# Kernel tuning notes

Hardware: AMD Instinct MI355X
Metric: run time of the kernel (lower is better)

## Reference

```python
import jax, jax.numpy as jnp
import numpy as np
from math import comb

LEVEL = 16
LENGTH = 64
TOPK = 2
SIZE = 512
BATCH = 32
NEG = -1e8


def _catalan(n_leaves):
    # number of distinct binary trees over n_leaves leaves
    m = n_leaves - 1
    return comb(2 * m, m) // (m + 1)


def _offsets(length, level):
    # cell offset of each chart level: level l occupies (length - l) cells
    return np.cumsum([0] + [length - l for l in range(level)])


def setup_inputs() -> dict:
    key = jax.random.key(0)
    K, B, size, level, length = TOPK, BATCH, SIZE, LEVEL, LENGTH
    L, N = length - level, level
    off = _offsets(length, level)
    ncells = int(off[-1])
    ks = jax.random.split(key, 5)
    chart_h = jax.random.normal(ks[0], (K, B, ncells, size), jnp.float32)
    chart_s = jax.random.normal(ks[1], (K, B, ncells, 1), jnp.float32)
    mat = jax.random.normal(ks[2], (size, size), jnp.float32) / np.sqrt(size).astype(np.float32)
    Wc = jax.random.normal(ks[3], (2 * size, size), jnp.float32) / np.sqrt(2 * size).astype(np.float32)
    bc = jnp.zeros((size,), jnp.float32)
    # structural gather indices: left child = (level n, pos), right child = (level level-1-n, pos+n+1)
    l_idx = np.zeros((L, N), np.int64)
    r_idx = np.zeros((L, N), np.int64)
    for pos in range(L):
        for n in range(N):
            l_idx[pos, n] = off[n] + pos
            r_idx[pos, n] = off[level - 1 - n] + pos + n + 1
    return {
        'chart_h': chart_h, 'chart_s': chart_s,
        'l_index': jnp.asarray(l_idx.reshape(-1)), 'r_index': jnp.asarray(r_idx.reshape(-1)),
        'mat': mat, 'Wc': Wc, 'bc': bc,
    }


def _penalty_mask(level, N, K):
    # Faithful to penalize_incomplete_splits: idx = i // K**2 == 0 for i < K*K,
    # so only the n_idx==0 block is ever penalized. l_level=0, r_level=level-1.
    M = N * K * K
    mask = np.zeros(M, bool)
    for i in range(K * K):
        lk, rk = i // K, i % K
        if _catalan(0 + 1) < lk + 1 or _catalan((level - 1) + 1) < rk + 1:
            mask[i] = True
    return jnp.asarray(mask)


def reference(chart_h, chart_s, l_index, r_index, mat, Wc, bc):
    K, B, ncells, size = chart_h.shape
    level = LEVEL
    N = level
    L = l_index.shape[0] // N
    M = N * K * K
    # gather child states from charts: (K,B,L,N,size) -> (B,L,N,K,size)
    lh = jnp.moveaxis(chart_h[:, :, l_index].reshape(K, B, L, N, size), 0, 3)
    rh = jnp.moveaxis(chart_h[:, :, r_index].reshape(K, B, L, N, size), 0, 3)
    ls = jnp.moveaxis(chart_s[:, :, l_index].reshape(K, B, L, N), 0, 3)  # (B,L,N,K)
    rs = jnp.moveaxis(chart_s[:, :, r_index].reshape(K, B, L, N), 0, 3)
    # bilinear composition score: (B,L,N,K_l,K_r)
    s_raw = jnp.einsum('blnkd,de,blnje->blnkj', lh, mat, rh)
    # flat combo index = n*K*K + lk*K + rk; add child scores
    s = (s_raw + ls[..., :, None] + rs[..., None, :]).reshape(B, L, M)
    s = jnp.where(_penalty_mask(level, N, K), jnp.float32(NEG), s)
    topk_s, topk_idx = jax.lax.top_k(s, K)  # (B,L,K), sorted descending like torch.topk
    # dense compose over all N*K*K combos
    combo_lh = jnp.repeat(lh, K, axis=3).reshape(B, L, M, size)   # lk = z // K
    combo_rh = jnp.tile(rh, (1, 1, 1, K, 1)).reshape(B, L, M, size)  # rk = z % K
    all_h = jnp.tanh(jnp.concatenate([combo_lh, combo_rh], axis=-1) @ Wc + bc)
    topk_h = jnp.take_along_axis(all_h, topk_idx[..., None], axis=2)  # (B,L,K,size)
    # UnitNorm normalize_func
    topk_h = topk_h / jnp.linalg.norm(topk_h, axis=-1, keepdims=True)
    topk_s = topk_s[..., None]  # (B,L,K,1) to match torch shape
    if _catalan(N + 1) < K:  # static no-op at this level
        topk_s = topk_s.at[:, :, _catalan(N + 1):].set(NEG)
    topk_n_idx = topk_idx // (K * K)
    topk_lk = (topk_idx % (K * K)) // K
    topk_rk = (topk_idx % (K * K)) % K
    return topk_h, topk_s, topk_n_idx, topk_lk, topk_rk
```

## Files before the change

kernel.cpp:

```cpp
#include <hip/hip_runtime.h>
#include <cstdint>
#include <cstddef>

#define B_DIM   32
#define L_DIM   48
#define NCELLS  904
#define SZ      512
#define NEGF    (-1e8f)
#define DELTA   0.25f
#define MAXC    32

#define OFF_S   1572864
#define OFF_N   1575936
#define OFF_L   1579008
#define OFF_R   1582080

typedef _Float16  f16x8 __attribute__((ext_vector_type(8)));
typedef float     f32x4 __attribute__((ext_vector_type(4)));

static __device__ __forceinline__ uint16_t f2bf(float f) {
    uint32_t u = __builtin_bit_cast(uint32_t, f);
    u += 0x7fffu + ((u >> 16) & 1u);
    return (uint16_t)(u >> 16);
}

#define GLD16(gp, lp) __builtin_amdgcn_global_load_lds(                        \
        (__attribute__((address_space(1))) void*)(gp),                         \
        (__attribute__((address_space(3))) void*)(lp), 16, 0, 0)

static __device__ __forceinline__ int level_off(int n) {
    return n * 64 - (n * (n - 1)) / 2;
}

__global__ __launch_bounds__(256)
void prep_mat(const float* __restrict__ mat, _Float16* __restrict__ P)
{
    const int tg   = blockIdx.x * 256 + threadIdx.x;
    const int c    = tg >> 6, lane = tg & 63;
    const int srow = 16 * (c & 31) + (lane & 15);
    const int scol = 32 * (c >> 5) + (lane >> 4) * 8;
    const float4 a = *(const float4*)(mat + (size_t)srow * 512 + scol);
    const float4 b = *(const float4*)(mat + (size_t)srow * 512 + scol + 4);
    f16x8 w;
    w[0]=(_Float16)(a.x*64.f); w[1]=(_Float16)(a.y*64.f);
    w[2]=(_Float16)(a.z*64.f); w[3]=(_Float16)(a.w*64.f);
    w[4]=(_Float16)(b.x*64.f); w[5]=(_Float16)(b.y*64.f);
    w[6]=(_Float16)(b.z*64.f); w[7]=(_Float16)(b.w*64.f);
    *(f16x8*)(P + (size_t)tg * 8) = w;
}

__global__ __launch_bounds__(256, 2)
void gemm_fused(const float* __restrict__ A,
                const _Float16* __restrict__ P,
                _Float16* __restrict__ C)
{
    __shared__ _Float16 As16[64 * 512];

    const int t = threadIdx.x;
    const int wave = t >> 6, lane = t & 63;
    const int n0 = blockIdx.x * 256;
    const int nq = n0 >> 4;
    const int m0 = blockIdx.y * 64;
    const int col_l = lane & 15, quad = lane >> 4;

    {
        const int r  = lane;
        const int cw = wave;
        const float* ap = A + (size_t)(m0 + r) * 512 + cw * 128;
        _Float16* drow = As16 + r * 512;
        const int swz = r & 7;
#pragma unroll 2
        for (int s = 0; s < 8; ++s) {
            const f32x4 a0 = *(const f32x4*)(ap + s * 16);
            const f32x4 a1 = *(const f32x4*)(ap + s * 16 + 4);
            const f32x4 a2 = *(const f32x4*)(ap + s * 16 + 8);
            const f32x4 a3 = *(const f32x4*)(ap + s * 16 + 12);
            f16x8 v0, v1;
#pragma unroll
            for (int j = 0; j < 4; ++j) {
                v0[j]     = (_Float16)(a0[j] * 16.f);
                v0[j + 4] = (_Float16)(a1[j] * 16.f);
                v1[j]     = (_Float16)(a2[j] * 16.f);
                v1[j + 4] = (_Float16)(a3[j] * 16.f);
            }
            const int u0 = cw * 16 + s * 2;
            *(f16x8*)&drow[(u0 ^ swz) * 8]       = v0;
            *(f16x8*)&drow[((u0 + 1) ^ swz) * 8] = v1;
        }
    }
    __syncthreads();

    f32x4 acc[4][4];
#pragma unroll
    for (int i = 0; i < 4; ++i)
#pragma unroll
        for (int j = 0; j < 4; ++j) acc[i][j] = (f32x4){0.f, 0.f, 0.f, 0.f};

#pragma unroll 4
    for (int w16 = 0; w16 < 16; ++w16) {
        f16x8 af[4];
#pragma unroll
        for (int mi = 0; mi < 4; ++mi) {
            const int r = mi * 16 + col_l;
            const int u = w16 * 4 + quad;
            af[mi] = *(const f16x8*)&As16[r * 512 + (u ^ (r & 7)) * 8];
        }
#pragma unroll
        for (int ni = 0; ni < 4; ++ni) {
            const int c = w16 * 32 + nq + wave * 4 + ni;
            const f16x8 bf = *(const f16x8*)(P + (size_t)c * 512 + lane * 8);
#pragma unroll
            for (int mi = 0; mi < 4; ++mi)
                acc[mi][ni] = __builtin_amdgcn_mfma_f32_16x16x32_f16(
                    af[mi], bf, acc[mi][ni], 0, 0, 0);
        }
    }

#pragma unroll
    for (int ni = 0; ni < 4; ++ni) {
        const int ncol = n0 + wave * 64 + ni * 16 + col_l;
#pragma unroll
        for (int mi = 0; mi < 4; ++mi) {
            const int mrow = m0 + mi * 16 + quad * 4;
#pragma unroll
            for (int r = 0; r < 4; ++r)
                C[(size_t)(mrow + r) * 512 + ncol] = (_Float16)acc[mi][ni][r];
        }
    }
}

static __device__ __forceinline__ void emit_outputs(
    int row, int i1, int i2, float v1, float v2, float* out)
{
    out[OFF_S + row * 2 + 0] = v1;
    out[OFF_S + row * 2 + 1] = v2;
    out[OFF_N + row * 2 + 0] = (float)(i1 >> 2);
    out[OFF_N + row * 2 + 1] = (float)(i2 >> 2);
    out[OFF_L + row * 2 + 0] = (float)((i1 >> 1) & 1);
    out[OFF_L + row * 2 + 1] = (float)((i2 >> 1) & 1);
    out[OFF_R + row * 2 + 0] = (float)(i1 & 1);
    out[OFF_R + row * 2 + 1] = (float)(i2 & 1);
}

static __device__ __forceinline__ void gather_x(
    int row, int pos, int b, const int* top_z,
    const float* __restrict__ chart_h, uint16_t* __restrict__ X, int tid)
{
#pragma unroll
    for (int kq = 0; kq < 2; ++kq) {
        const int z = top_z[kq];
        const int n = z >> 2, lk = (z >> 1) & 1, rk = z & 1;
        const int lcell = level_off(n) + pos;
        const int rcell = level_off(15 - n) + pos + n + 1;
        const float* srcl = chart_h + ((size_t)(lk * B_DIM + b) * NCELLS + lcell) * SZ;
        const float* srcr = chart_h + ((size_t)(rk * B_DIM + b) * NCELLS + rcell) * SZ;
        uint16_t* dst = X + ((size_t)row * 2 + kq) * 1024;
        const int e = tid * 2;
        const float2 a = *(const float2*)(srcl + e);
        const float2 c = *(const float2*)(srcr + e);
        *(uint32_t*)(dst + e)       = (uint32_t)f2bf(a.x) | ((uint32_t)f2bf(a.y) << 16);
        *(uint32_t*)(dst + 512 + e) = (uint32_t)f2bf(c.x) | ((uint32_t)f2bf(c.y) << 16);
    }
}

__global__ __launch_bounds__(256)
void score_topk(const float* __restrict__ chart_h,
                const _Float16* __restrict__ T16,
                const float* __restrict__ chart_s,
                uint32_t* __restrict__ items,
                int* __restrict__ rowbase,
                int* __restrict__ counter,
                int* __restrict__ flags,
                uint16_t* __restrict__ X,
                float* __restrict__ out)
{
    const int b   = blockIdx.x / L_DIM;
    const int pos = blockIdx.x % L_DIM;
    const int row = blockIdx.x;
    const int wave = threadIdx.x >> 6, lane = threadIdx.x & 63;

    __shared__ float s_sh[64];
    __shared__ int top_z[2];
    __shared__ int flag_sh;

#pragma unroll
    for (int ni = 0; ni < 4; ++ni) {
        const int n = wave * 4 + ni;
        const int lcell = level_off(n) + pos;
        const int rcell = level_off(15 - n) + pos + n + 1;

        const float* lp0 = chart_h + ((size_t)(0 * B_DIM + b) * NCELLS + lcell) * SZ + lane * 8;
        const float* lp1 = chart_h + ((size_t)(1 * B_DIM + b) * NCELLS + lcell) * SZ + lane * 8;
        const float4 l0a = *(const float4*)lp0, l0b = *(const float4*)(lp0 + 4);
        const float4 l1a = *(const float4*)lp1, l1b = *(const float4*)(lp1 + 4);
        const f16x8 t0 = *(const f16x8*)(T16 + ((size_t)(0 * B_DIM + b) * NCELLS + rcell) * SZ + lane * 8);
        const f16x8 t1 = *(const f16x8*)(T16 + ((size_t)(1 * B_DIM + b) * NCELLS + rcell) * SZ + lane * 8);

        float l0[8] = {l0a.x, l0a.y, l0a.z, l0a.w, l0b.x, l0b.y, l0b.z, l0b.w};
        float l1[8] = {l1a.x, l1a.y, l1a.z, l1a.w, l1b.x, l1b.y, l1b.z, l1b.w};

        float d00 = 0.f, d01 = 0.f, d10 = 0.f, d11 = 0.f;
#pragma unroll
        for (int j = 0; j < 8; ++j) {
            const float c0 = (float)t0[j], c1 = (float)t1[j];
            d00 += l0[j] * c0; d01 += l0[j] * c1;
            d10 += l1[j] * c0; d11 += l1[j] * c1;
        }
#pragma unroll
        for (int o = 32; o > 0; o >>= 1) {
            d00 += __shfl_down(d00, o);
            d01 += __shfl_down(d01, o);
            d10 += __shfl_down(d10, o);
            d11 += __shfl_down(d11, o);
        }
        if (lane == 0) {
            const float ls0 = chart_s[(size_t)(0 * B_DIM + b) * NCELLS + lcell];
            const float ls1 = chart_s[(size_t)(1 * B_DIM + b) * NCELLS + lcell];
            const float rs0 = chart_s[(size_t)(0 * B_DIM + b) * NCELLS + rcell];
            const float rs1 = chart_s[(size_t)(1 * B_DIM + b) * NCELLS + rcell];
            const float inv = 1.0f / 1024.0f;
            s_sh[n * 4 + 0] = d00 * inv + ls0 + rs0;
            s_sh[n * 4 + 1] = d01 * inv + ls0 + rs1;
            s_sh[n * 4 + 2] = d10 * inv + ls1 + rs0;
            s_sh[n * 4 + 3] = d11 * inv + ls1 + rs1;
        }
    }
    __syncthreads();

    if (threadIdx.x < 64) {
        float v = s_sh[lane];
        if (lane == 2 || lane == 3) v = NEGF;
        float v1 = v; int i1 = lane;
#pragma unroll
        for (int o = 32; o > 0; o >>= 1) {
            float ov = __shfl_down(v1, o);
            int   oi = __shfl_down(i1, o);
            if (ov > v1 || (ov == v1 && oi < i1)) { v1 = ov; i1 = oi; }
        }
        v1 = __shfl(v1, 0); i1 = __shfl(i1, 0);
        float v2 = (lane == i1) ? -3.4e38f : v; int i2 = lane;
#pragma unroll
        for (int o = 32; o > 0; o >>= 1) {
            float ov = __shfl_down(v2, o);
            int   oi = __shfl_down(i2, o);
            if (ov > v2 || (ov == v2 && oi < i2)) { v2 = ov; i2 = oi; }
        }
        v2 = __shfl(v2, 0); i2 = __shfl(i2, 0);
        float v3 = (lane == i1 || lane == i2) ? -3.4e38f : v;
#pragma unroll
        for (int o = 32; o > 0; o >>= 1) {
            const float ov = __shfl_down(v3, o);
            if (ov > v3) v3 = ov;
        }
        v3 = __shfl(v3, 0);

        const int f = (v1 - v2 < DELTA) || (v2 - v3 < DELTA);
        const bool cand = (v >= v2 - DELTA);
        const unsigned long long mask = __ballot(cand);
        const int nc_full = __popcll(mask);
        const int nc = nc_full < MAXC ? nc_full : MAXC;
        int base = 0;
        if (lane == 0) {
            flags[row] = f ? nc : 0;
            flag_sh = f;
            if (f) base = atomicAdd(counter, nc);
            rowbase[row] = base;
            top_z[0] = i1; top_z[1] = i2;
            if (!f) emit_outputs(row, i1, i2, v1, v2, out);
        }
        base = __shfl(base, 0);
        if (f && cand) {
            const int rank = __popcll(mask & ((1ull << lane) - 1ull));
            if (rank < MAXC) items[base + rank] = ((uint32_t)row << 6) | (uint32_t)lane;
        }
    }
    __syncthreads();

    if (!flag_sh)
        gather_x(row, pos, b, top_z, chart_h, X, threadIdx.x);
}

__global__ __launch_bounds__(256)
void refine_eval(const float* __restrict__ chart_h,
                 const float* __restrict__ chart_s,
                 const float* __restrict__ mat,
                 const uint32_t* __restrict__ items,
                 const int* __restrict__ counter,
                 float* __restrict__ exval)
{
    const int total = *counter;
    const int t = threadIdx.x;
    const int wave = t >> 6, lane = t & 63;

    __shared__ float lh_sh[2][512];
    __shared__ float psum[2][4];

    for (int p = blockIdx.x; 2 * p < total; p += gridDim.x) {
        const int it0 = 2 * p;
        const int it1v = (2 * p + 1 < total);
        const uint32_t item0 = items[it0];
        const uint32_t item1 = it1v ? items[it0 + 1] : item0;

        int rowA = item0 >> 6, zA = item0 & 63;
        int bA = rowA / L_DIM, posA = rowA % L_DIM;
        int nA = zA >> 2, lkA = (zA >> 1) & 1, rkA = zA & 1;
        int lcA = level_off(nA) + posA, rcA = level_off(15 - nA) + posA + nA + 1;
        int rowB = item1 >> 6, zB = item1 & 63;
        int bB = rowB / L_DIM, posB = rowB % L_DIM;
        int nB = zB >> 2, lkB = (zB >> 1) & 1, rkB = zB & 1;
        int lcB = level_off(nB) + posB, rcB = level_off(15 - nB) + posB + nB + 1;

        const float* lhA = chart_h + ((size_t)(lkA * B_DIM + bA) * NCELLS + lcA) * SZ;
        const float* rhA = chart_h + ((size_t)(rkA * B_DIM + bA) * NCELLS + rcA) * SZ;
        const float* lhB = chart_h + ((size_t)(lkB * B_DIM + bB) * NCELLS + lcB) * SZ;
        const float* rhB = chart_h + ((size_t)(rkB * B_DIM + bB) * NCELLS + rcB) * SZ;

        __syncthreads();
        lh_sh[0][t] = lhA[t]; lh_sh[0][t + 256] = lhA[t + 256];
        lh_sh[1][t] = lhB[t]; lh_sh[1][t + 256] = lhB[t + 256];
        const float4 rA0 = *(const float4*)(rhA + lane * 8);
        const float4 rA1 = *(const float4*)(rhA + lane * 8 + 4);
        const float4 rB0 = *(const float4*)(rhB + lane * 8);
        const float4 rB1 = *(const float4*)(rhB + lane * 8 + 4);
        __syncthreads();

        const float* mb = mat + (size_t)(wave * 128) * 512 + lane * 8;
        float a00 = 0.f, a01 = 0.f, b00 = 0.f, b01 = 0.f;
        for (int e = 0; e < 128; e += 2) {
            const float4 m0 = *(const float4*)(mb + (size_t)(e + 0) * 512);
            const float4 m1 = *(const float4*)(mb + (size_t)(e + 0) * 512 + 4);
            const float4 m2 = *(const float4*)(mb + (size_t)(e + 1) * 512);
            const float4 m3 = *(const float4*)(mb + (size_t)(e + 1) * 512 + 4);
            const int eg = wave * 128 + e;
            const float lA0 = lh_sh[0][eg],     lB0 = lh_sh[1][eg];
            const float lA1 = lh_sh[0][eg + 1], lB1 = lh_sh[1][eg + 1];
            const float dA0 = m0.x*rA0.x + m0.y*rA0.y + m0.z*rA0.z + m0.w*rA0.w
                            + m1.x*rA1.x + m1.y*rA1.y + m1.z*rA1.z + m1.w*rA1.w;
            const float dB0 = m0.x*rB0.x + m0.y*rB0.y + m0.z*rB0.z + m0.w*rB0.w
                            + m1.x*rB1.x + m1.y*rB1.y + m1.z*rB1.z + m1.w*rB1.w;
            const float dA1 = m2.x*rA0.x + m2.y*rA0.y + m2.z*rA0.z + m2.w*rA0.w
                            + m3.x*rA1.x + m3.y*rA1.y + m3.z*rA1.z + m3.w*rA1.w;
            const float dB1 = m2.x*rB0.x + m2.y*rB0.y + m2.z*rB0.z + m2.w*rB0.w
                            + m3.x*rB1.x + m3.y*rB1.y + m3.z*rB1.z + m3.w*rB1.w;
            a00 += lA0 * dA0; a01 += lA1 * dA1;
            b00 += lB0 * dB0; b01 += lB1 * dB1;
        }
        float sA = a00 + a01, sB = b00 + b01;
#pragma unroll
        for (int o = 32; o > 0; o >>= 1) {
            sA += __shfl_down(sA, o);
            sB += __shfl_down(sB, o);
        }
        if (lane == 0) { psum[0][wave] = sA; psum[1][wave] = sB; }
        __syncthreads();
        if (t == 0) {
            const float lsA = chart_s[(size_t)(lkA * B_DIM + bA) * NCELLS + lcA];
            const float rsA = chart_s[(size_t)(rkA * B_DIM + bA) * NCELLS + rcA];
            exval[it0] = psum[0][0] + psum[0][1] + psum[0][2] + psum[0][3] + lsA + rsA;
            if (it1v) {
                const float lsB = chart_s[(size_t)(lkB * B_DIM + bB) * NCELLS + lcB];
                const float rsB = chart_s[(size_t)(rkB * B_DIM + bB) * NCELLS + rcB];
                exval[it0 + 1] = psum[1][0] + psum[1][1] + psum[1][2] + psum[1][3] + lsB + rsB;
            }
        }
    }
}

__global__ __launch_bounds__(256)
void refine_pick(const float* __restrict__ chart_h,
                 const uint32_t* __restrict__ items,
                 const int* __restrict__ rowbase,
                 const int* __restrict__ flags,
                 const float* __restrict__ exval,
                 uint16_t* __restrict__ X,
                 float* __restrict__ out)
{
    const int row = blockIdx.x;
    const int nc = flags[row];
    if (nc == 0) return;
    const int b = row / L_DIM, pos = row % L_DIM;
    const int t = threadIdx.x;

    __shared__ int top_z[2];

    if (t == 0) {
        const int base = rowbase[row];
        float v1 = -3.4e38f; int c1 = -1;
        for (int c = 0; c < nc; ++c) {
            const float v = exval[base + c];
            if (v > v1) { v1 = v; c1 = c; }
        }
        float v2 = -3.4e38f; int c2 = -1;
        for (int c = 0; c < nc; ++c) {
            if (c == c1) continue;
            const float v = exval[base + c];
            if (v > v2) { v2 = v; c2 = c; }
        }
        const int i1 = (int)(items[base + c1] & 63u);
        const int i2 = (int)(items[base + c2] & 63u);
        top_z[0] = i1; top_z[1] = i2;
        emit_outputs(row, i1, i2, v1, v2, out);
    }
    __syncthreads();
    gather_x(row, pos, b, top_z, chart_h, X, t);
}

__global__ __launch_bounds__(256)
void transpose_wc(const float* __restrict__ Wc, uint16_t* __restrict__ WcT)
{
    __shared__ float tbuf[64][65];
    const int i0 = blockIdx.x * 64;
    const int o0 = blockIdx.y * 64;
    const int c = threadIdx.x & 63, r4 = threadIdx.x >> 6;
    for (int rr = r4; rr < 64; rr += 4)
        tbuf[rr][c] = Wc[(size_t)(i0 + rr) * 512 + o0 + c];
    __syncthreads();
    for (int rr = r4; rr < 64; rr += 4)
        WcT[(size_t)(o0 + rr) * 1024 + i0 + c] = f2bf(tbuf[c][rr]);
}

typedef __bf16 bf16x8 __attribute__((ext_vector_type(8)));

__global__ __launch_bounds__(256, 2)
void gemm_compose(const uint16_t* __restrict__ A,
                  const uint16_t* __restrict__ Bm,
                  const float* __restrict__ bias,
                  float* __restrict__ C,
                  int M, int Nn, int Kk)
{
    __shared__ uint16_t As[128 * 64];
    __shared__ uint16_t Bs[128 * 64];

    const int tid  = threadIdx.x;
    const int wave = tid >> 6, lane = tid & 63;
    const int m0 = blockIdx.x * 128, n0 = blockIdx.y * 128;
    const int wm = (wave & 1) * 64, wn = (wave >> 1) * 64;
    const int col_l = lane & 15, quad = lane >> 4;
    const int lrow = lane >> 3;
    const int lcol = (lane & 7) * 8;

    f32x4 acc[4][4];
#pragma unroll
    for (int i = 0; i < 4; ++i)
#pragma unroll
        for (int j = 0; j < 4; ++j) acc[i][j] = (f32x4){0.f, 0.f, 0.f, 0.f};

    for (int k0 = 0; k0 < Kk; k0 += 64) {
        __syncthreads();
#pragma unroll
        for (int i = 0; i < 4; ++i) {
            const int q = wave * 4 + i;
            const int r = q * 8 + lrow;
            GLD16(A  + (size_t)(m0 + r) * Kk + k0 + lcol, (char*)As + q * 1024);
            GLD16(Bm + (size_t)(n0 + r) * Kk + k0 + lcol, (char*)Bs + q * 1024);
        }
        __syncthreads();
#pragma unroll
        for (int kk = 0; kk < 64; kk += 32) {
            bf16x8 af[4], bfr[4];
#pragma unroll
            for (int mi = 0; mi < 4; ++mi)
                af[mi] = *(const bf16x8*)&As[(wm + mi * 16 + col_l) * 64 + kk + quad * 8];
#pragma unroll
            for (int ni = 0; ni < 4; ++ni)
                bfr[ni] = *(const bf16x8*)&Bs[(wn + ni * 16 + col_l) * 64 + kk + quad * 8];
#pragma unroll
            for (int mi = 0; mi < 4; ++mi)
#pragma unroll
                for (int ni = 0; ni < 4; ++ni)
                    acc[mi][ni] = __builtin_amdgcn_mfma_f32_16x16x32_bf16(
                        af[mi], bfr[ni], acc[mi][ni], 0, 0, 0);
        }
    }

#pragma unroll
    for (int ni = 0; ni < 4; ++ni) {
        const int ncol = n0 + wn + ni * 16 + col_l;
        const float bv = bias[ncol];
#pragma unroll
        for (int mi = 0; mi < 4; ++mi) {
            const int mrow = m0 + wm + mi * 16 + quad * 4;
#pragma unroll
            for (int r = 0; r < 4; ++r)
                C[(size_t)(mrow + r) * Nn + ncol] = tanhf(acc[mi][ni][r] + bv);
        }
    }
}

__global__ __launch_bounds__(256)
void norm_rows(const float* __restrict__ H, float* __restrict__ out)
{
    const int row = blockIdx.x;
    const float* h = H + (size_t)row * SZ;
    const int t = threadIdx.x;
    const int wave = t >> 6, lane = t & 63;
    const float a = h[t], c = h[t + 256];
    float ss = a * a + c * c;
#pragma unroll
    for (int o = 32; o > 0; o >>= 1) ss += __shfl_down(ss, o);
    __shared__ float wsum[4];
    if (lane == 0) wsum[wave] = ss;
    __syncthreads();
    const float inv = rsqrtf(wsum[0] + wsum[1] + wsum[2] + wsum[3]);
    out[(size_t)row * SZ + t]       = a * inv;
    out[(size_t)row * SZ + t + 256] = c * inv;
}

extern "C" void kernel_launch(void* const* d_in, const int* in_sizes, int n_in,
                              void* d_out, int out_size, void* d_ws, size_t ws_size,
                              hipStream_t stream)
{
    const float* chart_h = (const float*)d_in[0];
    const float* chart_s = (const float*)d_in[1];
    const float* mat = (const float*)d_in[4];
    const float* Wc  = (const float*)d_in[5];
    const float* bc  = (const float*)d_in[6];
    float* out = (float*)d_out;

    char* ws = (char*)d_ws;
    _Float16* T16   = (_Float16*)ws;
    _Float16* MAT16 = (_Float16*)(ws + 59244544);
    uint32_t* ITEMS = (uint32_t*)(ws + 59768832);
    float*    EXVAL = (float*)(ws + 59965440);
    int*      RBASE = (int*)(ws + 60162048);
    int*      CNT   = (int*)(ws + 60168192);
    int*      FLAGS = (int*)(ws + 60168448);
    uint16_t* X     = (uint16_t*)(ws + 60174592);
    uint16_t* WcT   = (uint16_t*)ws;
    float*    H     = (float*)(ws + 1048576);

    hipMemsetAsync(CNT, 0, 4, stream);
    prep_mat<<<dim3(128), 256, 0, stream>>>(mat, MAT16);
    gemm_fused<<<dim3(2, 904), 256, 0, stream>>>(chart_h, MAT16, T16);
    score_topk<<<dim3(B_DIM * L_DIM), 256, 0, stream>>>(chart_h, T16, chart_s,
                                                        ITEMS, RBASE, CNT, FLAGS, X, out);
    transpose_wc<<<dim3(16, 8), 256, 0, stream>>>(Wc, WcT);
    refine_eval<<<dim3(1024), 256, 0, stream>>>(chart_h, chart_s, mat, ITEMS, CNT, EXVAL);
    refine_pick<<<dim3(B_DIM * L_DIM), 256, 0, stream>>>(chart_h, ITEMS, RBASE, FLAGS,
                                                         EXVAL, X, out);
    gemm_compose<<<dim3(24, 4), 256, 0, stream>>>(X, WcT, bc, H, 3072, 512, 1024);
    norm_rows<<<dim3(3072), 256, 0, stream>>>(H, out);
}
```

Measured before the change: 322.2 us.

## Pre-convert chart_h to fp16 once and load it directly into GEMM LDS

Adds a standalone conversion kernel that writes the whole chart_h tensor as scaled fp16 into workspace. The GEMM then fills its LDS tile with direct global-to-LDS loads instead of converting fp32 inside each block, which previously happened twice because of the two column blocks. The scoring kernel also reads fp16 left children, which halves its load bytes. In exchange there is an extra full pass over chart_h (read fp32, write fp16) plus lower score precision, which could change top-k picks near ties.

```diff
diff --git a/kernel.cpp b/kernel.cpp
--- a/kernel.cpp
+++ b/kernel.cpp
@@ -49,8 +49,22 @@
     *(f16x8*)(P + (size_t)tg * 8) = w;
 }
 
+__global__ __launch_bounds__(256)
+void conv_h(const float* __restrict__ x, _Float16* __restrict__ y)
+{
+    const size_t i = ((size_t)blockIdx.x * 256 + threadIdx.x) * 8;
+    const float4 a = *(const float4*)(x + i);
+    const float4 b = *(const float4*)(x + i + 4);
+    f16x8 w;
+    w[0]=(_Float16)(a.x*16.f); w[1]=(_Float16)(a.y*16.f);
+    w[2]=(_Float16)(a.z*16.f); w[3]=(_Float16)(a.w*16.f);
+    w[4]=(_Float16)(b.x*16.f); w[5]=(_Float16)(b.y*16.f);
+    w[6]=(_Float16)(b.z*16.f); w[7]=(_Float16)(b.w*16.f);
+    *(f16x8*)(y + i) = w;
+}
+
 __global__ __launch_bounds__(256, 2)
-void gemm_fused(const float* __restrict__ A,
+void gemm_fused(const _Float16* __restrict__ A16,
                 const _Float16* __restrict__ P,
                 _Float16* __restrict__ C)
 {
@@ -63,30 +77,11 @@
     const int m0 = blockIdx.y * 64;
     const int col_l = lane & 15, quad = lane >> 4;
 
-    {
-        const int r  = lane;
-        const int cw = wave;
-        const float* ap = A + (size_t)(m0 + r) * 512 + cw * 128;
-        _Float16* drow = As16 + r * 512;
-        const int swz = r & 7;
-#pragma unroll 2
-        for (int s = 0; s < 8; ++s) {
-            const f32x4 a0 = *(const f32x4*)(ap + s * 16);
-            const f32x4 a1 = *(const f32x4*)(ap + s * 16 + 4);
-            const f32x4 a2 = *(const f32x4*)(ap + s * 16 + 8);
-            const f32x4 a3 = *(const f32x4*)(ap + s * 16 + 12);
-            f16x8 v0, v1;
-#pragma unroll
-            for (int j = 0; j < 4; ++j) {
-                v0[j]     = (_Float16)(a0[j] * 16.f);
-                v0[j + 4] = (_Float16)(a1[j] * 16.f);
-                v1[j]     = (_Float16)(a2[j] * 16.f);
-                v1[j + 4] = (_Float16)(a3[j] * 16.f);
-            }
-            const int u0 = cw * 16 + s * 2;
-            *(f16x8*)&drow[(u0 ^ swz) * 8]       = v0;
-            *(f16x8*)&drow[((u0 + 1) ^ swz) * 8] = v1;
-        }
+#pragma unroll
+    for (int i = 0; i < 16; ++i) {
+        const int r = wave * 16 + i;
+        GLD16(A16 + (size_t)(m0 + r) * 512 + ((lane ^ (r & 7)) * 8),
+              (char*)As16 + r * 1024);
     }
     __syncthreads();
 
@@ -165,6 +160,7 @@
 
 __global__ __launch_bounds__(256)
 void score_topk(const float* __restrict__ chart_h,
+                const _Float16* __restrict__ CH16,
                 const _Float16* __restrict__ T16,
                 const float* __restrict__ chart_s,
                 uint32_t* __restrict__ items,
@@ -189,22 +185,18 @@
         const int lcell = level_off(n) + pos;
         const int rcell = level_off(15 - n) + pos + n + 1;
 
-        const float* lp0 = chart_h + ((size_t)(0 * B_DIM + b) * NCELLS + lcell) * SZ + lane * 8;
-        const float* lp1 = chart_h + ((size_t)(1 * B_DIM + b) * NCELLS + lcell) * SZ + lane * 8;
-        const float4 l0a = *(const float4*)lp0, l0b = *(const float4*)(lp0 + 4);
-        const float4 l1a = *(const float4*)lp1, l1b = *(const float4*)(lp1 + 4);
+        const f16x8 lv0 = *(const f16x8*)(CH16 + ((size_t)(0 * B_DIM + b) * NCELLS + lcell) * SZ + lane * 8);
+        const f16x8 lv1 = *(const f16x8*)(CH16 + ((size_t)(1 * B_DIM + b) * NCELLS + lcell) * SZ + lane * 8);
         const f16x8 t0 = *(const f16x8*)(T16 + ((size_t)(0 * B_DIM + b) * NCELLS + rcell) * SZ + lane * 8);
         const f16x8 t1 = *(const f16x8*)(T16 + ((size_t)(1 * B_DIM + b) * NCELLS + rcell) * SZ + lane * 8);
 
-        float l0[8] = {l0a.x, l0a.y, l0a.z, l0a.w, l0b.x, l0b.y, l0b.z, l0b.w};
-        float l1[8] = {l1a.x, l1a.y, l1a.z, l1a.w, l1b.x, l1b.y, l1b.z, l1b.w};
-
         float d00 = 0.f, d01 = 0.f, d10 = 0.f, d11 = 0.f;
 #pragma unroll
         for (int j = 0; j < 8; ++j) {
             const float c0 = (float)t0[j], c1 = (float)t1[j];
-            d00 += l0[j] * c0; d01 += l0[j] * c1;
-            d10 += l1[j] * c0; d11 += l1[j] * c1;
+            const float l0 = (float)lv0[j], l1 = (float)lv1[j];
+            d00 += l0 * c0; d01 += l0 * c1;
+            d10 += l1 * c0; d11 += l1 * c1;
         }
 #pragma unroll
         for (int o = 32; o > 0; o >>= 1) {
@@ -218,7 +210,7 @@
             const float ls1 = chart_s[(size_t)(1 * B_DIM + b) * NCELLS + lcell];
             const float rs0 = chart_s[(size_t)(0 * B_DIM + b) * NCELLS + rcell];
             const float rs1 = chart_s[(size_t)(1 * B_DIM + b) * NCELLS + rcell];
-            const float inv = 1.0f / 1024.0f;
+            const float inv = 1.0f / 16384.0f;
             s_sh[n * 4 + 0] = d00 * inv + ls0 + rs0;
             s_sh[n * 4 + 1] = d01 * inv + ls0 + rs1;
             s_sh[n * 4 + 2] = d10 * inv + ls1 + rs0;
@@ -526,13 +518,15 @@
     int*      CNT   = (int*)(ws + 60168192);
     int*      FLAGS = (int*)(ws + 60168448);
     uint16_t* X     = (uint16_t*)(ws + 60174592);
+    _Float16* CH16  = (_Float16*)(ws + 66466048);
     uint16_t* WcT   = (uint16_t*)ws;
     float*    H     = (float*)(ws + 1048576);
 
     hipMemsetAsync(CNT, 0, 4, stream);
     prep_mat<<<dim3(128), 256, 0, stream>>>(mat, MAT16);
-    gemm_fused<<<dim3(2, 904), 256, 0, stream>>>(chart_h, MAT16, T16);
-    score_topk<<<dim3(B_DIM * L_DIM), 256, 0, stream>>>(chart_h, T16, chart_s,
+    conv_h<<<dim3(14464), 256, 0, stream>>>(chart_h, CH16);
+    gemm_fused<<<dim3(2, 904), 256, 0, stream>>>(CH16, MAT16, T16);
+    score_topk<<<dim3(B_DIM * L_DIM), 256, 0, stream>>>(chart_h, CH16, T16, chart_s,
                                                         ITEMS, RBASE, CNT, FLAGS, X, out);
     transpose_wc<<<dim3(16, 8), 256, 0, stream>>>(Wc, WcT);
     refine_eval<<<dim3(1024), 256, 0, stream>>>(chart_h, chart_s, mat, ITEMS, CNT, EXVAL);
```

Result: slower. 341.6 us (+6.0%).
